# Performance work log

Measured on AMD Instinct MI355X. Metric: run time of the kernel, lower is better.

## Reference

```python
import jax, jax.numpy as jnp
import numpy as np
import math

MAX_T = 1000

def _timestep_emb(t, emb_dim):
    half = emb_dim // 2
    freqs = jnp.exp(jnp.arange(half, dtype=jnp.float32) * -(math.log(MAX_T) / (half - 1)))
    e = t.astype(jnp.float32)[:, None] * freqs[None, :]
    return jnp.concatenate([jnp.sin(e), jnp.cos(e)], axis=1)  # [bs, emb_dim]


def setup_inputs() -> dict:
    key = jax.random.key(0)
    ks = jax.random.split(key, 12)
    BS, N, D, H = 16, 1024, 128, 8  # batch, nodes(=in_channels), out_dim(=d), heads
    w = lambda k, shape: jax.random.normal(k, shape, dtype=jnp.float32) * 0.05
    return {
        "A_t": jax.random.normal(ks[0], (BS, N, N), dtype=jnp.float32),
        "F_c": jax.random.normal(ks[1], (BS, N, D), dtype=jnp.float32),
        "t": jax.random.randint(ks[2], (BS,), 0, MAX_T),
        "Wq": w(ks[3], (D, D * H)), "bq": jnp.zeros((D * H,), jnp.float32),
        "Wk": w(ks[4], (D, D * H)), "bk": jnp.zeros((D * H,), jnp.float32),
        "Wv": w(ks[5], (D, D * H)), "bv": jnp.zeros((D * H,), jnp.float32),
        "Wo": w(ks[6], (D * H, D)), "bo": jnp.zeros((D,), jnp.float32),
        "Wg": jnp.eye(D, dtype=jnp.float32),  # GCN weight, eye init
    }


def reference(A_t, F_c, t, Wq, bq, Wk, bk, Wv, bv, Wo, bo, Wg):
    BS, N, D = F_c.shape
    H = Wq.shape[1] // D
    # timestep embedding, emb_dim = in_channels = N
    t_emb = _timestep_emb(t, N)                       # [bs, N]
    c = F_c + t_emb[:, :, None]                       # [bs, N, D]
    # naive multi-head self-attention with per-head dim = out_dim
    q = (c @ Wq + bq).reshape(BS, N, H, D).transpose(0, 2, 1, 3)
    k = (c @ Wk + bk).reshape(BS, N, H, D).transpose(0, 2, 1, 3)
    v = (c @ Wv + bv).reshape(BS, N, H, D).transpose(0, 2, 1, 3)
    scores = jnp.einsum('bhnd,bhmd->bhnm', q, k) / math.sqrt(D)
    a = jax.nn.softmax(scores, axis=-1)
    ctx = jnp.einsum('bhnm,bhmd->bhnd', a, v)
    ctx = ctx.transpose(0, 2, 1, 3).reshape(BS, N, H * D)
    h = ctx @ Wo + bo                                 # [bs, N, D]
    # GCN: relu(A @ (h @ W))
    feat = jax.nn.relu(A_t @ (h @ Wg))                # [bs, N, D]
    # Corr: row-normalize (unbiased std, matching torch.std) then bmm
    mu = feat.mean(axis=-1, keepdims=True)
    std = jnp.std(feat, axis=-1, ddof=1, keepdims=True)
    norm = (feat - mu) / (std + 1e-8)
    return jnp.einsum('bnd,bmd->bnm', norm, norm) / feat.shape[-1]
```

## Files before the change

kernel.cpp:

```cpp
#include <hip/hip_runtime.h>
#include <math.h>

#define NN 1024
#define DD 128
#define HH 8

typedef __attribute__((ext_vector_type(8))) short short8;
typedef __attribute__((ext_vector_type(4))) float f32x4;

__device__ inline unsigned short f2bf(float x) {
    union { float f; unsigned u; } v; v.f = x;
    return (unsigned short)((v.u + 0x7FFF + ((v.u >> 16) & 1)) >> 16);
}
__device__ inline unsigned pack2(float a, float b) {
    return (unsigned)f2bf(a) | ((unsigned)f2bf(b) << 16);
}

__global__ __launch_bounds__(256) void k_prep_w(
    const float* __restrict__ Wq, const float* __restrict__ Wk, const float* __restrict__ Wv,
    const float* __restrict__ Wo, const float* __restrict__ Wg,
    unsigned short* WqT, unsigned short* WkT, unsigned short* WvT,
    unsigned short* WoT, unsigned short* WgT) {
    int id = blockIdx.x;
    const float* src; unsigned short* dst; int R, C, ti;
    if (id < 128)      { src = Wq; dst = WqT; R = 128;  C = 1024; ti = id; }
    else if (id < 256) { src = Wk; dst = WkT; R = 128;  C = 1024; ti = id - 128; }
    else if (id < 384) { src = Wv; dst = WvT; R = 128;  C = 1024; ti = id - 256; }
    else if (id < 512) { src = Wo; dst = WoT; R = 1024; C = 128;  ti = id - 384; }
    else               { src = Wg; dst = WgT; R = 128;  C = 128;  ti = id - 512; }
    int tc = C >> 5;
    int r0 = (ti / tc) << 5, c0 = (ti % tc) << 5;
    __shared__ float T[32][33];
    int tid = threadIdx.x;
    int r = tid >> 3, c4 = (tid & 7) << 2;
    float4 v = *(const float4*)&src[(size_t)(r0 + r) * C + c0 + c4];
    T[r][c4] = v.x; T[r][c4 + 1] = v.y; T[r][c4 + 2] = v.z; T[r][c4 + 3] = v.w;
    __syncthreads();
    int c = tid >> 3, r4 = (tid & 7) << 2;
    uint2 o;
    o.x = pack2(T[r4][c], T[r4 + 1][c]);
    o.y = pack2(T[r4 + 2][c], T[r4 + 3][c]);
    *(uint2*)&dst[(size_t)(c0 + c) * R + r0 + r4] = o;
}

__global__ __launch_bounds__(256) void k_embed(const float* __restrict__ F_c,
                                               const int* __restrict__ t,
                                               unsigned short* __restrict__ cb) {
    int gi = blockIdx.x * 256 + threadIdx.x;
    int row = gi >> 4, ch = gi & 15;
    int b = row >> 10, n = row & 1023;
    float tv = (float)t[b];
    int j = n & 511;
    float e = tv * expf(-(float)j * 0.013518112092919054f);
    float emb = (n < 512) ? sinf(e) : cosf(e);
    const float* src = F_c + (size_t)row * 128 + ch * 8;
    float4 a = *(const float4*)src;
    float4 c4 = *(const float4*)(src + 4);
    uint4 o;
    o.x = pack2(a.x + emb, a.y + emb);  o.y = pack2(a.z + emb, a.w + emb);
    o.z = pack2(c4.x + emb, c4.y + emb); o.w = pack2(c4.z + emb, c4.w + emb);
    *(uint4*)&cb[(size_t)row * 128 + ch * 8] = o;
}

__device__ __forceinline__ void proj_body(const unsigned short* __restrict__ Ain,
                                          const unsigned short* __restrict__ WT,
                                          const float* __restrict__ bias,
                                          unsigned short* __restrict__ Out,
                                          float scale, int mode, int bh_mul,
                                          unsigned short* sm, int head, int m0) {
    unsigned short* CT  = sm;
    unsigned short* WTs = sm + 128 * 136;
    int tid = threadIdx.x;
    int w = tid >> 6, lane = tid & 63, n16 = lane & 15, quad = lane >> 4;
#pragma unroll
    for (int p = 0; p < 8; ++p) {
        int idx = tid + p * 256;
        int r = idx >> 4, ch = idx & 15;
        *(uint4*)&CT[r * 136 + ch * 8]  = *(const uint4*)&Ain[(size_t)(m0 + r) * 128 + ch * 8];
        *(uint4*)&WTs[r * 136 + ch * 8] = *(const uint4*)&WT[(size_t)(head * 128 + r) * 128 + ch * 8];
    }
    __syncthreads();
    int wr = (w >> 1) * 64, wc = (w & 1) * 64;
    f32x4 acc[4][4];
#pragma unroll
    for (int i = 0; i < 4; i++)
#pragma unroll
        for (int j = 0; j < 4; j++) acc[i][j] = (f32x4){0.f, 0.f, 0.f, 0.f};
#pragma unroll
    for (int kk = 0; kk < 4; ++kk) {
        short8 af[4], bf[4];
#pragma unroll
        for (int rb = 0; rb < 4; ++rb)
            af[rb] = *(const short8*)&CT[(wr + rb * 16 + n16) * 136 + kk * 32 + quad * 8];
#pragma unroll
        for (int cb = 0; cb < 4; ++cb)
            bf[cb] = *(const short8*)&WTs[(wc + cb * 16 + n16) * 136 + kk * 32 + quad * 8];
#pragma unroll
        for (int rb = 0; rb < 4; ++rb)
#pragma unroll
            for (int cb = 0; cb < 4; ++cb)
                acc[rb][cb] = __builtin_amdgcn_mfma_f32_16x16x32_bf16(af[rb], bf[cb], acc[rb][cb], 0, 0, 0);
    }
    __syncthreads();
#pragma unroll
    for (int rb = 0; rb < 4; ++rb)
#pragma unroll
        for (int cb = 0; cb < 4; ++cb) {
            int colb = wc + cb * 16 + n16;
            float bs = bias ? bias[head * 128 + colb] : 0.f;
#pragma unroll
            for (int reg = 0; reg < 4; ++reg) {
                int rowb = wr + rb * 16 + quad * 4 + reg;
                unsigned short val = f2bf((acc[rb][cb][reg] + bs) * scale);
                if (mode == 0) CT[rowb * 136 + colb] = val;
                else           CT[colb * 136 + rowb] = val;
            }
        }
    __syncthreads();
    int b = m0 >> 10, n0 = m0 & 1023;
    size_t base = (size_t)(b * bh_mul + head) * 131072;
    if (mode == 0) {
#pragma unroll
        for (int p = 0; p < 8; ++p) {
            int idx = tid + p * 256;
            int r = idx >> 4, ch = idx & 15;
            *(uint4*)&Out[base + (size_t)(n0 + r) * 128 + ch * 8] = *(const uint4*)&CT[r * 136 + ch * 8];
        }
    } else {
#pragma unroll
        for (int p = 0; p < 8; ++p) {
            int idx = tid + p * 256;
            int r = idx >> 4, ch = idx & 15;
            *(uint4*)&Out[base + (size_t)r * 1024 + n0 + ch * 8] = *(const uint4*)&CT[r * 136 + ch * 8];
        }
    }
}

__global__ __launch_bounds__(256) void k_proj_qkv(const unsigned short* __restrict__ Ain,
                                                  const unsigned short* __restrict__ W0,
                                                  const unsigned short* __restrict__ W1,
                                                  const unsigned short* __restrict__ W2,
                                                  const float* __restrict__ b0,
                                                  const float* __restrict__ b1,
                                                  const float* __restrict__ b2,
                                                  unsigned short* __restrict__ O0,
                                                  unsigned short* __restrict__ O1,
                                                  unsigned short* __restrict__ O2,
                                                  float qscale) {
    __shared__ __align__(16) unsigned short sm[2 * 128 * 136];
    int z = blockIdx.z;
    const unsigned short* WT = (z == 0) ? W0 : (z == 1) ? W1 : W2;
    const float* bias = (z == 0) ? b0 : (z == 1) ? b1 : b2;
    unsigned short* Out = (z == 0) ? O0 : (z == 1) ? O1 : O2;
    float scale = (z == 0) ? qscale : 1.f;
    int mode = (z == 2) ? 1 : 0;
    proj_body(Ain, WT, bias, Out, scale, mode, 8, sm, blockIdx.y, blockIdx.x * 128);
}

__global__ __launch_bounds__(256) void k_proj(const unsigned short* __restrict__ Ain,
                                              const unsigned short* __restrict__ WT,
                                              const float* __restrict__ bias,
                                              unsigned short* __restrict__ Out,
                                              float scale, int mode, int bh_mul) {
    __shared__ __align__(16) unsigned short sm[2 * 128 * 136];
    proj_body(Ain, WT, bias, Out, scale, mode, bh_mul, sm, blockIdx.y, blockIdx.x * 128);
}

__device__ __forceinline__ void attn_compute(const unsigned short* __restrict__ Ksc,
                                             const unsigned short* __restrict__ Vtc,
                                             const short8 (&qf)[2][4],
                                             float (&mrun)[2], float (&lrun)[2],
                                             f32x4 (&O)[2][8], int n16, int quad) {
    f32x4 S[2][4];
#pragma unroll
    for (int qb2 = 0; qb2 < 2; ++qb2)
#pragma unroll
        for (int kb = 0; kb < 4; ++kb) S[qb2][kb] = (f32x4){0.f, 0.f, 0.f, 0.f};
    __builtin_amdgcn_s_setprio(1);
#pragma unroll
    for (int kb = 0; kb < 4; ++kb)
#pragma unroll
        for (int dc = 0; dc < 4; ++dc) {
            short8 kf = *(const short8*)&Ksc[(kb * 16 + n16) * 136 + dc * 32 + quad * 8];
            S[0][kb] = __builtin_amdgcn_mfma_f32_16x16x32_bf16(kf, qf[0][dc], S[0][kb], 0, 0, 0);
            S[1][kb] = __builtin_amdgcn_mfma_f32_16x16x32_bf16(kf, qf[1][dc], S[1][kb], 0, 0, 0);
        }
    __builtin_amdgcn_s_setprio(0);

    float mx[2];
#pragma unroll
    for (int qb2 = 0; qb2 < 2; ++qb2) {
        float m = S[qb2][0][0];
#pragma unroll
        for (int kb = 0; kb < 4; ++kb)
#pragma unroll
            for (int reg = 0; reg < 4; ++reg) m = fmaxf(m, S[qb2][kb][reg]);
        m = fmaxf(m, __shfl_xor(m, 16));
        m = fmaxf(m, __shfl_xor(m, 32));
        mx[qb2] = m;
    }
    int keep = (mx[0] - mrun[0] <= 1.f) && (mx[1] - mrun[1] <= 1.f);
    if (!__all(keep)) {
        float mn0 = fmaxf(mrun[0], mx[0]);
        float mn1 = fmaxf(mrun[1], mx[1]);
        float a0 = __expf(mrun[0] - mn0);
        float a1 = __expf(mrun[1] - mn1);
        mrun[0] = mn0; mrun[1] = mn1;
        lrun[0] *= a0; lrun[1] *= a1;
        float av0[4], av1[4];
#pragma unroll
        for (int reg = 0; reg < 4; ++reg) {
            av0[reg] = __shfl(a0, quad * 4 + reg);
            av1[reg] = __shfl(a1, quad * 4 + reg);
        }
#pragma unroll
        for (int dc = 0; dc < 8; ++dc)
#pragma unroll
            for (int reg = 0; reg < 4; ++reg) {
                O[0][dc][reg] *= av0[reg];
                O[1][dc][reg] *= av1[reg];
            }
    }
#pragma unroll
    for (int qb2 = 0; qb2 < 2; ++qb2) {
        float ps = 0.f;
#pragma unroll
        for (int kb = 0; kb < 4; ++kb)
#pragma unroll
            for (int reg = 0; reg < 4; ++reg) {
                float p = __expf(S[qb2][kb][reg] - mrun[qb2]);
                S[qb2][kb][reg] = p;
                ps += p;
            }
        ps += __shfl_xor(ps, 16);
        ps += __shfl_xor(ps, 32);
        lrun[qb2] += ps;
    }
    unsigned pk01[2][4], pk23[2][4];
#pragma unroll
    for (int qb2 = 0; qb2 < 2; ++qb2)
#pragma unroll
        for (int kb = 0; kb < 4; ++kb) {
            asm("v_cvt_pk_bf16_f32 %0, %1, %2"
                : "=v"(pk01[qb2][kb]) : "v"(S[qb2][kb][0]), "v"(S[qb2][kb][1]));
            asm("v_cvt_pk_bf16_f32 %0, %1, %2"
                : "=v"(pk23[qb2][kb]) : "v"(S[qb2][kb][2]), "v"(S[qb2][kb][3]));
        }
    __builtin_amdgcn_s_setprio(1);
#pragma unroll
    for (int c = 0; c < 2; ++c) {
        union { uint4 u; short8 s; } pa0, pa1;
        pa0.u = make_uint4(pk01[0][2 * c], pk23[0][2 * c], pk01[0][2 * c + 1], pk23[0][2 * c + 1]);
        pa1.u = make_uint4(pk01[1][2 * c], pk23[1][2 * c], pk01[1][2 * c + 1], pk23[1][2 * c + 1]);
#pragma unroll
        for (int dc = 0; dc < 8; ++dc) {
            short8 vf = *(const short8*)&Vtc[(dc * 16 + n16) * 72 + c * 32 + quad * 8];
            O[0][dc] = __builtin_amdgcn_mfma_f32_16x16x32_bf16(pa0.s, vf, O[0][dc], 0, 0, 0);
            O[1][dc] = __builtin_amdgcn_mfma_f32_16x16x32_bf16(pa1.s, vf, O[1][dc], 0, 0, 0);
        }
    }
    __builtin_amdgcn_s_setprio(0);
}

__global__ __launch_bounds__(256, 2) void k_attn2(const unsigned short* __restrict__ qbuf,
                                                  const unsigned short* __restrict__ kbuf,
                                                  const unsigned short* __restrict__ vtb,
                                                  unsigned short* __restrict__ ctxb) {
    __shared__ __align__(16) unsigned short sm[35840];
    const int tid = threadIdx.x;
    const int w = tid >> 6, lane = tid & 63;
    const int n16 = lane & 15, quad = lane >> 4;
    const int g = blockIdx.x;
    const int bh = g & 127, tileq = g >> 7;

    const unsigned short* Qp = qbuf + (size_t)bh * 131072 + (size_t)tileq * 16384;
    const unsigned short* Kp = kbuf + (size_t)bh * 131072;
    const unsigned short* Vp = vtb + (size_t)bh * 131072;

    short8 qf[2][4];
#pragma unroll
    for (int qb2 = 0; qb2 < 2; ++qb2)
#pragma unroll
        for (int dc = 0; dc < 4; ++dc)
            qf[qb2][dc] = *(const short8*)&Qp[(size_t)(w * 32 + qb2 * 16 + n16) * 128 + dc * 32 + quad * 8];

    float mrun[2] = {-1e30f, -1e30f};
    float lrun[2] = {0.f, 0.f};
    f32x4 O[2][8];
#pragma unroll
    for (int qb2 = 0; qb2 < 2; ++qb2)
#pragma unroll
        for (int dc = 0; dc < 8; ++dc) O[qb2][dc] = (f32x4){0.f, 0.f, 0.f, 0.f};

    const int vr0 = tid >> 3;
    const int k0 = (tid & 7) * 8;
    const int slotA = ((k0 >> 5) << 5) | (((k0 >> 2) & 3) << 3) | (((k0 >> 4) & 1) << 2);

    uint4 ka[4], va[4];
#pragma unroll
    for (int p = 0; p < 4; ++p) {
        int idx = tid + p * 256;
        int r = idx >> 4, ch = idx & 15;
        ka[p] = *(const uint4*)&Kp[(size_t)r * 128 + ch * 8];
        va[p] = *(const uint4*)&Vp[(size_t)(vr0 + p * 32) * 1024 + k0];
    }
    {
        unsigned short* Kw = sm;
        unsigned short* Vw = sm + 8704;
#pragma unroll
        for (int p = 0; p < 4; ++p) {
            int idx = tid + p * 256;
            int r = idx >> 4, ch = idx & 15;
            *(uint4*)&Kw[r * 136 + ch * 8] = ka[p];
        }
#pragma unroll
        for (int p = 0; p < 4; ++p) {
            int r = vr0 + p * 32;
            *(uint2*)&Vw[r * 72 + slotA]     = make_uint2(va[p].x, va[p].y);
            *(uint2*)&Vw[r * 72 + slotA + 8] = make_uint2(va[p].z, va[p].w);
        }
    }
    __syncthreads();

    for (int kt = 0; kt < 16; ++kt) {
        if (kt < 15) {
#pragma unroll
            for (int p = 0; p < 4; ++p) {
                int idx = tid + p * 256;
                int r = idx >> 4, ch = idx & 15;
                ka[p] = *(const uint4*)&Kp[(size_t)((kt + 1) * 64 + r) * 128 + ch * 8];
                va[p] = *(const uint4*)&Vp[(size_t)(vr0 + p * 32) * 1024 + (kt + 1) * 64 + k0];
            }
        }
        {
            const unsigned short* Ksc = sm + (kt & 1) * 17920;
            const unsigned short* Vtc = Ksc + 8704;
            attn_compute(Ksc, Vtc, qf, mrun, lrun, O, n16, quad);
        }
        if (kt < 15) {
            unsigned short* Kw = sm + ((kt + 1) & 1) * 17920;
            unsigned short* Vw = Kw + 8704;
#pragma unroll
            for (int p = 0; p < 4; ++p) {
                int idx = tid + p * 256;
                int r = idx >> 4, ch = idx & 15;
                *(uint4*)&Kw[r * 136 + ch * 8] = ka[p];
            }
#pragma unroll
            for (int p = 0; p < 4; ++p) {
                int r = vr0 + p * 32;
                *(uint2*)&Vw[r * 72 + slotA]     = make_uint2(va[p].x, va[p].y);
                *(uint2*)&Vw[r * 72 + slotA + 8] = make_uint2(va[p].z, va[p].w);
            }
        }
        __syncthreads();
    }

    float lv[2][4];
#pragma unroll
    for (int qb2 = 0; qb2 < 2; ++qb2)
#pragma unroll
        for (int reg = 0; reg < 4; ++reg)
            lv[qb2][reg] = 1.f / __shfl(lrun[qb2], quad * 4 + reg);
    unsigned short* Ct = sm;
#pragma unroll
    for (int qb2 = 0; qb2 < 2; ++qb2)
#pragma unroll
        for (int reg = 0; reg < 4; ++reg) {
            int row = w * 32 + qb2 * 16 + quad * 4 + reg;
#pragma unroll
            for (int dc = 0; dc < 8; ++dc)
                Ct[row * 136 + dc * 16 + n16] = f2bf(O[qb2][dc][reg] * lv[qb2][reg]);
        }
    __syncthreads();
    unsigned short* Outp = ctxb + (size_t)bh * 131072 + (size_t)tileq * 16384;
#pragma unroll
    for (int p = 0; p < 8; ++p) {
        int idx = tid + p * 256;
        int r = idx >> 4, ch = idx & 15;
        *(uint4*)&Outp[(size_t)r * 128 + ch * 8] = *(const uint4*)&Ct[r * 136 + ch * 8];
    }
}

__global__ __launch_bounds__(256) void k_proj_o(const unsigned short* __restrict__ Ctxb,
                                                const unsigned short* __restrict__ WoT,
                                                const float* __restrict__ bo,
                                                unsigned short* __restrict__ Hb) {
    __shared__ __align__(16) unsigned short sm[64 * 72 + 128 * 72];
    unsigned short* As = sm;
    unsigned short* Bs = sm + 64 * 72;
    int tid = threadIdx.x;
    int m0 = blockIdx.x * 64;
    int b = m0 >> 10, n0 = m0 & 1023;
    int w = tid >> 6, lane = tid & 63, n16 = lane & 15, quad = lane >> 4;
    int wr = (w & 1) * 32, wc = (w >> 1) * 64;
    f32x4 acc[2][4];
#pragma unroll
    for (int i = 0; i < 2; i++)
#pragma unroll
        for (int j = 0; j < 4; j++) acc[i][j] = (f32x4){0.f, 0.f, 0.f, 0.f};
    for (int kt = 0; kt < 16; ++kt) {
        __syncthreads();
        int hh = kt >> 1, d0 = (kt & 1) * 64;
#pragma unroll
        for (int p = 0; p < 2; ++p) {
            int idx = tid + p * 256;
            int r = idx >> 3, ch = idx & 7;
            *(uint4*)&As[r * 72 + ch * 8] =
                *(const uint4*)&Ctxb[((size_t)(b * 8 + hh) * 1024 + n0 + r) * 128 + d0 + ch * 8];
        }
#pragma unroll
        for (int p = 0; p < 4; ++p) {
            int idx = tid + p * 256;
            int r = idx >> 3, ch = idx & 7;
            *(uint4*)&Bs[r * 72 + ch * 8] = *(const uint4*)&WoT[(size_t)r * 1024 + kt * 64 + ch * 8];
        }
        __syncthreads();
#pragma unroll
        for (int kk = 0; kk < 2; ++kk) {
            short8 af0 = *(const short8*)&As[(wr + n16) * 72 + kk * 32 + quad * 8];
            short8 af1 = *(const short8*)&As[(wr + 16 + n16) * 72 + kk * 32 + quad * 8];
#pragma unroll
            for (int cb = 0; cb < 4; ++cb) {
                short8 bf = *(const short8*)&Bs[(wc + cb * 16 + n16) * 72 + kk * 32 + quad * 8];
                acc[0][cb] = __builtin_amdgcn_mfma_f32_16x16x32_bf16(af0, bf, acc[0][cb], 0, 0, 0);
                acc[1][cb] = __builtin_amdgcn_mfma_f32_16x16x32_bf16(af1, bf, acc[1][cb], 0, 0, 0);
            }
        }
    }
    __syncthreads();
    unsigned short* Ct = sm;
#pragma unroll
    for (int rb = 0; rb < 2; ++rb)
#pragma unroll
        for (int cb = 0; cb < 4; ++cb) {
            int col = wc + cb * 16 + n16;
            float bs = bo[col];
#pragma unroll
            for (int reg = 0; reg < 4; ++reg)
                Ct[(wr + rb * 16 + quad * 4 + reg) * 136 + col] = f2bf(acc[rb][cb][reg] + bs);
        }
    __syncthreads();
#pragma unroll
    for (int p = 0; p < 4; ++p) {
        int idx = tid + p * 256;
        int r = idx >> 4, ch = idx & 15;
        *(uint4*)&Hb[(size_t)(m0 + r) * 128 + ch * 8] = *(const uint4*)&Ct[r * 136 + ch * 8];
    }
}

__global__ __launch_bounds__(256) void k_at_gemm(const float* __restrict__ At,
                                                 const unsigned short* __restrict__ HgT,
                                                 float* __restrict__ Feat) {
    __shared__ __align__(16) unsigned short sm[64 * 72 + 128 * 72];
    unsigned short* As = sm;
    unsigned short* Bs = sm + 64 * 72;
    int tid = threadIdx.x;
    int bz = blockIdx.z;
    int m0 = blockIdx.x * 64;
    int w = tid >> 6, lane = tid & 63, n16 = lane & 15, quad = lane >> 4;
    int wr = (w & 1) * 32, wc = (w >> 1) * 64;
    f32x4 acc[2][4];
#pragma unroll
    for (int i = 0; i < 2; i++)
#pragma unroll
        for (int j = 0; j < 4; j++) acc[i][j] = (f32x4){0.f, 0.f, 0.f, 0.f};
    for (int kt = 0; kt < 16; ++kt) {
        __syncthreads();
#pragma unroll
        for (int p = 0; p < 2; ++p) {
            int idx = tid + p * 256;
            int r = idx >> 3, ch = idx & 7;
            const float* s = At + (size_t)bz * 1048576 + (size_t)(m0 + r) * 1024 + kt * 64 + ch * 8;
            float4 x = *(const float4*)s;
            float4 y = *(const float4*)(s + 4);
            uint4 o;
            o.x = pack2(x.x, x.y); o.y = pack2(x.z, x.w);
            o.z = pack2(y.x, y.y); o.w = pack2(y.z, y.w);
            *(uint4*)&As[r * 72 + ch * 8] = o;
        }
#pragma unroll
        for (int p = 0; p < 4; ++p) {
            int idx = tid + p * 256;
            int r = idx >> 3, ch = idx & 7;
            *(uint4*)&Bs[r * 72 + ch * 8] =
                *(const uint4*)&HgT[(size_t)bz * 131072 + (size_t)r * 1024 + kt * 64 + ch * 8];
        }
        __syncthreads();
#pragma unroll
        for (int kk = 0; kk < 2; ++kk) {
            short8 af0 = *(const short8*)&As[(wr + n16) * 72 + kk * 32 + quad * 8];
            short8 af1 = *(const short8*)&As[(wr + 16 + n16) * 72 + kk * 32 + quad * 8];
#pragma unroll
            for (int cb = 0; cb < 4; ++cb) {
                short8 bf = *(const short8*)&Bs[(wc + cb * 16 + n16) * 72 + kk * 32 + quad * 8];
                acc[0][cb] = __builtin_amdgcn_mfma_f32_16x16x32_bf16(af0, bf, acc[0][cb], 0, 0, 0);
                acc[1][cb] = __builtin_amdgcn_mfma_f32_16x16x32_bf16(af1, bf, acc[1][cb], 0, 0, 0);
            }
        }
    }
#pragma unroll
    for (int rb = 0; rb < 2; ++rb)
#pragma unroll
        for (int cb = 0; cb < 4; ++cb) {
            int col = wc + cb * 16 + n16;
#pragma unroll
            for (int reg = 0; reg < 4; ++reg) {
                int row = m0 + wr + rb * 16 + quad * 4 + reg;
                Feat[(size_t)bz * 131072 + (size_t)row * 128 + col] = fmaxf(acc[rb][cb][reg], 0.f);
            }
        }
}

__global__ __launch_bounds__(64) void k_norm(const float* __restrict__ F,
                                             unsigned short* __restrict__ Nb) {
    int row = blockIdx.x, tdx = threadIdx.x;
    const float* p = F + (size_t)row * 128;
    float2 xy = *(const float2*)&p[tdx * 2];
    float sum = xy.x + xy.y;
#pragma unroll
    for (int off = 32; off; off >>= 1) sum += __shfl_xor(sum, off);
    float mu = sum * (1.f / 128.f);
    float d0 = xy.x - mu, d1 = xy.y - mu;
    float sq = d0 * d0 + d1 * d1;
#pragma unroll
    for (int off = 32; off; off >>= 1) sq += __shfl_xor(sq, off);
    float sd = sqrtf(sq * (1.f / 127.f));
    float inv = 1.f / (sd + 1e-8f);
    ((unsigned*)Nb)[(size_t)row * 64 + tdx] = pack2(d0 * inv, d1 * inv);
}

__global__ __launch_bounds__(256) void k_corr(const unsigned short* __restrict__ Nb,
                                              float* __restrict__ Out) {
    __shared__ __align__(16) unsigned short sm[2 * 128 * 136];
    unsigned short* Ar = sm;
    unsigned short* Br = sm + 128 * 136;
    int tid = threadIdx.x;
    int bz = blockIdx.z;
    int n0 = blockIdx.x * 128, m0 = blockIdx.y * 128;
    const unsigned short* base = Nb + (size_t)bz * 131072;
    int w = tid >> 6, lane = tid & 63, n16 = lane & 15, quad = lane >> 4;
#pragma unroll
    for (int p = 0; p < 8; ++p) {
        int idx = tid + p * 256;
        int r = idx >> 4, ch = idx & 15;
        *(uint4*)&Ar[r * 136 + ch * 8] = *(const uint4*)&base[(size_t)(n0 + r) * 128 + ch * 8];
        *(uint4*)&Br[r * 136 + ch * 8] = *(const uint4*)&base[(size_t)(m0 + r) * 128 + ch * 8];
    }
    __syncthreads();
    int wr = (w >> 1) * 64, wc = (w & 1) * 64;
    f32x4 acc[4][4];
#pragma unroll
    for (int i = 0; i < 4; i++)
#pragma unroll
        for (int j = 0; j < 4; j++) acc[i][j] = (f32x4){0.f, 0.f, 0.f, 0.f};
#pragma unroll
    for (int kk = 0; kk < 4; ++kk) {
        short8 af[4], bf[4];
#pragma unroll
        for (int rb = 0; rb < 4; ++rb)
            af[rb] = *(const short8*)&Ar[(wr + rb * 16 + n16) * 136 + kk * 32 + quad * 8];
#pragma unroll
        for (int cb = 0; cb < 4; ++cb)
            bf[cb] = *(const short8*)&Br[(wc + cb * 16 + n16) * 136 + kk * 32 + quad * 8];
#pragma unroll
        for (int rb = 0; rb < 4; ++rb)
#pragma unroll
            for (int cb = 0; cb < 4; ++cb)
                acc[rb][cb] = __builtin_amdgcn_mfma_f32_16x16x32_bf16(af[rb], bf[cb], acc[rb][cb], 0, 0, 0);
    }
#pragma unroll
    for (int rb = 0; rb < 4; ++rb)
#pragma unroll
        for (int cb = 0; cb < 4; ++cb)
#pragma unroll
            for (int reg = 0; reg < 4; ++reg) {
                int row = n0 + wr + rb * 16 + quad * 4 + reg;
                int col = m0 + wc + cb * 16 + n16;
                Out[(size_t)bz * 1048576 + (size_t)row * 1024 + col] = acc[rb][cb][reg] * 0.0078125f;
            }
}

extern "C" void kernel_launch(void* const* d_in, const int* in_sizes, int n_in,
                              void* d_out, int out_size, void* d_ws, size_t ws_size,
                              hipStream_t stream) {
    const float* A_t = (const float*)d_in[0];
    const float* F_c = (const float*)d_in[1];
    const int*   t   = (const int*)d_in[2];
    const float* Wq  = (const float*)d_in[3];
    const float* bq  = (const float*)d_in[4];
    const float* Wk  = (const float*)d_in[5];
    const float* bk  = (const float*)d_in[6];
    const float* Wv  = (const float*)d_in[7];
    const float* bv  = (const float*)d_in[8];
    const float* Wo  = (const float*)d_in[9];
    const float* bo  = (const float*)d_in[10];
    const float* Wg  = (const float*)d_in[11];
    float* out = (float*)d_out;
    char* ws = (char*)d_ws;

    unsigned short* cb   = (unsigned short*)(ws);
    unsigned short* qb   = (unsigned short*)(ws + 4194304);
    unsigned short* kbuf = (unsigned short*)(ws + 37748736);
    unsigned short* vtb  = (unsigned short*)(ws + 71303168);
    unsigned short* ctxb = (unsigned short*)(ws + 104857600);
    unsigned short* hb   = (unsigned short*)(ws + 138412032);
    unsigned short* hgT  = (unsigned short*)(ws + 142606336);
    float*          feat = (float*)        (ws + 146800640);
    unsigned short* nb   = (unsigned short*)(ws + 155189248);
    unsigned short* WqT  = (unsigned short*)(ws + 159383552);
    unsigned short* WkT  = (unsigned short*)(ws + 159645696);
    unsigned short* WvT  = (unsigned short*)(ws + 159907840);
    unsigned short* WoT  = (unsigned short*)(ws + 160169984);
    unsigned short* WgT  = (unsigned short*)(ws + 160432128);

    const float qscale = 0.08838834764831845f;

    k_prep_w<<<528, 256, 0, stream>>>(Wq, Wk, Wv, Wo, Wg, WqT, WkT, WvT, WoT, WgT);
    k_embed<<<1024, 256, 0, stream>>>(F_c, t, cb);
    k_proj_qkv<<<dim3(128, 8, 3), 256, 0, stream>>>(cb, WqT, WkT, WvT, bq, bk, bv,
                                                    qb, kbuf, vtb, qscale);
    k_attn2<<<1024, 256, 0, stream>>>(qb, kbuf, vtb, ctxb);
    k_proj_o<<<256, 256, 0, stream>>>(ctxb, WoT, bo, hb);
    k_proj<<<dim3(128, 1), 256, 0, stream>>>(hb, WgT, nullptr, hgT, 1.f, 1, 1);
    k_at_gemm<<<dim3(16, 1, 16), 256, 0, stream>>>(A_t, hgT, feat);
    k_norm<<<16384, 64, 0, stream>>>(feat, nb);
    k_corr<<<dim3(8, 8, 16), 256, 0, stream>>>(nb, out);
}
```

Before: 348.5 us.

## Swizzle attention K/V LDS layout and double-buffer out-proj and adjacency GEMMs

The attention kernel drops padded LDS row strides for K and V^T and uses XOR-swizzled unpadded layouts. This cuts LDS to 64KB per block and is meant to avoid bank conflicts without padding. The output-projection and A_t GEMM kernels gain register-staged double buffering: the next tile's global loads are issued before the current tile's MFMAs, so each k-step needs one barrier instead of two. This doubles their shared memory and adds register pressure, which may cost occupancy.

Result: faster. 321.6 us (-7.7%).

```diff
diff --git a/kernel.cpp b/kernel.cpp
--- a/kernel.cpp
+++ b/kernel.cpp
@@ -171,6 +171,7 @@
                                              const short8 (&qf)[2][4],
                                              float (&mrun)[2], float (&lrun)[2],
                                              f32x4 (&O)[2][8], int n16, int quad) {
+    const int swz = (n16 & 7) << 3;
     f32x4 S[2][4];
 #pragma unroll
     for (int qb2 = 0; qb2 < 2; ++qb2)
@@ -181,7 +182,7 @@
     for (int kb = 0; kb < 4; ++kb)
 #pragma unroll
         for (int dc = 0; dc < 4; ++dc) {
-            short8 kf = *(const short8*)&Ksc[(kb * 16 + n16) * 136 + dc * 32 + quad * 8];
+            short8 kf = *(const short8*)&Ksc[((kb * 16 + n16) << 7) + ((dc * 32 + quad * 8) ^ swz)];
             S[0][kb] = __builtin_amdgcn_mfma_f32_16x16x32_bf16(kf, qf[0][dc], S[0][kb], 0, 0, 0);
             S[1][kb] = __builtin_amdgcn_mfma_f32_16x16x32_bf16(kf, qf[1][dc], S[1][kb], 0, 0, 0);
         }
@@ -254,7 +255,7 @@
         pa1.u = make_uint4(pk01[1][2 * c], pk23[1][2 * c], pk01[1][2 * c + 1], pk23[1][2 * c + 1]);
 #pragma unroll
         for (int dc = 0; dc < 8; ++dc) {
-            short8 vf = *(const short8*)&Vtc[(dc * 16 + n16) * 72 + c * 32 + quad * 8];
+            short8 vf = *(const short8*)&Vtc[((dc * 16 + n16) << 6) + ((c * 32 + quad * 8) ^ swz)];
             O[0][dc] = __builtin_amdgcn_mfma_f32_16x16x32_bf16(pa0.s, vf, O[0][dc], 0, 0, 0);
             O[1][dc] = __builtin_amdgcn_mfma_f32_16x16x32_bf16(pa1.s, vf, O[1][dc], 0, 0, 0);
         }
@@ -266,7 +267,7 @@
                                                   const unsigned short* __restrict__ kbuf,
                                                   const unsigned short* __restrict__ vtb,
                                                   unsigned short* __restrict__ ctxb) {
-    __shared__ __align__(16) unsigned short sm[35840];
+    __shared__ __align__(16) unsigned short sm[32768];
     const int tid = threadIdx.x;
     const int w = tid >> 6, lane = tid & 63;
     const int n16 = lane & 15, quad = lane >> 4;
@@ -295,29 +296,27 @@
     const int vr0 = tid >> 3;
     const int k0 = (tid & 7) * 8;
     const int slotA = ((k0 >> 5) << 5) | (((k0 >> 2) & 3) << 3) | (((k0 >> 4) & 1) << 2);
+    const int voff = slotA ^ ((vr0 & 7) << 3);
+    const int kr0 = tid >> 4, kch = tid & 15;
+    const int kwoff = ((kch ^ (kr0 & 7)) << 3);
 
     uint4 ka[4], va[4];
 #pragma unroll
     for (int p = 0; p < 4; ++p) {
-        int idx = tid + p * 256;
-        int r = idx >> 4, ch = idx & 15;
-        ka[p] = *(const uint4*)&Kp[(size_t)r * 128 + ch * 8];
+        ka[p] = *(const uint4*)&Kp[(size_t)(kr0 + p * 16) * 128 + kch * 8];
         va[p] = *(const uint4*)&Vp[(size_t)(vr0 + p * 32) * 1024 + k0];
     }
     {
         unsigned short* Kw = sm;
-        unsigned short* Vw = sm + 8704;
+        unsigned short* Vw = sm + 8192;
+#pragma unroll
+        for (int p = 0; p < 4; ++p)
+            *(uint4*)&Kw[((kr0 + p * 16) << 7) + kwoff] = ka[p];
 #pragma unroll
         for (int p = 0; p < 4; ++p) {
-            int idx = tid + p * 256;
-            int r = idx >> 4, ch = idx & 15;
-            *(uint4*)&Kw[r * 136 + ch * 8] = ka[p];
-        }
-#pragma unroll
-        for (int p = 0; p < 4; ++p) {
-            int r = vr0 + p * 32;
-            *(uint2*)&Vw[r * 72 + slotA]     = make_uint2(va[p].x, va[p].y);
-            *(uint2*)&Vw[r * 72 + slotA + 8] = make_uint2(va[p].z, va[p].w);
+            int rb6 = (vr0 + p * 32) << 6;
+            *(uint2*)&Vw[rb6 + voff]       = make_uint2(va[p].x, va[p].y);
+            *(uint2*)&Vw[rb6 + (voff ^ 8)] = make_uint2(va[p].z, va[p].w);
         }
     }
     __syncthreads();
@@ -326,31 +325,26 @@
         if (kt < 15) {
 #pragma unroll
             for (int p = 0; p < 4; ++p) {
-                int idx = tid + p * 256;
-                int r = idx >> 4, ch = idx & 15;
-                ka[p] = *(const uint4*)&Kp[(size_t)((kt + 1) * 64 + r) * 128 + ch * 8];
+                ka[p] = *(const uint4*)&Kp[(size_t)((kt + 1) * 64 + kr0 + p * 16) * 128 + kch * 8];
                 va[p] = *(const uint4*)&Vp[(size_t)(vr0 + p * 32) * 1024 + (kt + 1) * 64 + k0];
             }
         }
         {
-            const unsigned short* Ksc = sm + (kt & 1) * 17920;
-            const unsigned short* Vtc = Ksc + 8704;
+            const unsigned short* Ksc = sm + (kt & 1) * 16384;
+            const unsigned short* Vtc = Ksc + 8192;
             attn_compute(Ksc, Vtc, qf, mrun, lrun, O, n16, quad);
         }
         if (kt < 15) {
-            unsigned short* Kw = sm + ((kt + 1) & 1) * 17920;
-            unsigned short* Vw = Kw + 8704;
+            unsigned short* Kw = sm + ((kt + 1) & 1) * 16384;
+            unsigned short* Vw = Kw + 8192;
+#pragma unroll
+            for (int p = 0; p < 4; ++p)
+                *(uint4*)&Kw[((kr0 + p * 16) << 7) + kwoff] = ka[p];
 #pragma unroll
             for (int p = 0; p < 4; ++p) {
-                int idx = tid + p * 256;
-                int r = idx >> 4, ch = idx & 15;
-                *(uint4*)&Kw[r * 136 + ch * 8] = ka[p];
-            }
-#pragma unroll
-            for (int p = 0; p < 4; ++p) {
-                int r = vr0 + p * 32;
-                *(uint2*)&Vw[r * 72 + slotA]     = make_uint2(va[p].x, va[p].y);
-                *(uint2*)&Vw[r * 72 + slotA + 8] = make_uint2(va[p].z, va[p].w);
+                int rb6 = (vr0 + p * 32) << 6;
+                *(uint2*)&Vw[rb6 + voff]       = make_uint2(va[p].x, va[p].y);
+                *(uint2*)&Vw[rb6 + (voff ^ 8)] = make_uint2(va[p].z, va[p].w);
             }
         }
         __syncthreads();
@@ -386,36 +380,46 @@
                                                 const unsigned short* __restrict__ WoT,
                                                 const float* __restrict__ bo,
                                                 unsigned short* __restrict__ Hb) {
-    __shared__ __align__(16) unsigned short sm[64 * 72 + 128 * 72];
-    unsigned short* As = sm;
-    unsigned short* Bs = sm + 64 * 72;
+    __shared__ __align__(16) unsigned short sm[2 * 13824];
     int tid = threadIdx.x;
     int m0 = blockIdx.x * 64;
     int b = m0 >> 10, n0 = m0 & 1023;
     int w = tid >> 6, lane = tid & 63, n16 = lane & 15, quad = lane >> 4;
     int wr = (w & 1) * 32, wc = (w >> 1) * 64;
+    int r8 = tid >> 3, ch8 = tid & 7;
     f32x4 acc[2][4];
 #pragma unroll
     for (int i = 0; i < 2; i++)
 #pragma unroll
         for (int j = 0; j < 4; j++) acc[i][j] = (f32x4){0.f, 0.f, 0.f, 0.f};
+    uint4 aR[2], bR[4];
+#pragma unroll
+    for (int p = 0; p < 2; ++p)
+        aR[p] = *(const uint4*)&Ctxb[((size_t)(b * 8) * 1024 + n0 + r8 + p * 32) * 128 + ch8 * 8];
+#pragma unroll
+    for (int p = 0; p < 4; ++p)
+        bR[p] = *(const uint4*)&WoT[(size_t)(r8 + p * 32) * 1024 + ch8 * 8];
+    {
+        unsigned short* As = sm;
+        unsigned short* Bs = sm + 64 * 72;
+#pragma unroll
+        for (int p = 0; p < 2; ++p) *(uint4*)&As[(r8 + p * 32) * 72 + ch8 * 8] = aR[p];
+#pragma unroll
+        for (int p = 0; p < 4; ++p) *(uint4*)&Bs[(r8 + p * 32) * 72 + ch8 * 8] = bR[p];
+    }
+    __syncthreads();
     for (int kt = 0; kt < 16; ++kt) {
-        __syncthreads();
-        int hh = kt >> 1, d0 = (kt & 1) * 64;
-#pragma unroll
-        for (int p = 0; p < 2; ++p) {
-            int idx = tid + p * 256;
-            int r = idx >> 3, ch = idx & 7;
-            *(uint4*)&As[r * 72 + ch * 8] =
-                *(const uint4*)&Ctxb[((size_t)(b * 8 + hh) * 1024 + n0 + r) * 128 + d0 + ch * 8];
-        }
-#pragma unroll
-        for (int p = 0; p < 4; ++p) {
-            int idx = tid + p * 256;
-            int r = idx >> 3, ch = idx & 7;
-            *(uint4*)&Bs[r * 72 + ch * 8] = *(const uint4*)&WoT[(size_t)r * 1024 + kt * 64 + ch * 8];
-        }
-        __syncthreads();
+        if (kt < 15) {
+            int kn = kt + 1, hh = kn >> 1, d0 = (kn & 1) * 64;
+#pragma unroll
+            for (int p = 0; p < 2; ++p)
+                aR[p] = *(const uint4*)&Ctxb[((size_t)(b * 8 + hh) * 1024 + n0 + r8 + p * 32) * 128 + d0 + ch8 * 8];
+#pragma unroll
+            for (int p = 0; p < 4; ++p)
+                bR[p] = *(const uint4*)&WoT[(size_t)(r8 + p * 32) * 1024 + kn * 64 + ch8 * 8];
+        }
+        const unsigned short* As = sm + (kt & 1) * 13824;
+        const unsigned short* Bs = As + 64 * 72;
 #pragma unroll
         for (int kk = 0; kk < 2; ++kk) {
             short8 af0 = *(const short8*)&As[(wr + n16) * 72 + kk * 32 + quad * 8];
@@ -427,8 +431,16 @@
                 acc[1][cb] = __builtin_amdgcn_mfma_f32_16x16x32_bf16(af1, bf, acc[1][cb], 0, 0, 0);
             }
         }
-    }
-    __syncthreads();
+        if (kt < 15) {
+            unsigned short* Aw = sm + ((kt + 1) & 1) * 13824;
+            unsigned short* Bw = Aw + 64 * 72;
+#pragma unroll
+            for (int p = 0; p < 2; ++p) *(uint4*)&Aw[(r8 + p * 32) * 72 + ch8 * 8] = aR[p];
+#pragma unroll
+            for (int p = 0; p < 4; ++p) *(uint4*)&Bw[(r8 + p * 32) * 72 + ch8 * 8] = bR[p];
+        }
+        __syncthreads();
+    }
     unsigned short* Ct = sm;
 #pragma unroll
     for (int rb = 0; rb < 2; ++rb)
@@ -452,41 +464,57 @@
 __global__ __launch_bounds__(256) void k_at_gemm(const float* __restrict__ At,
                                                  const unsigned short* __restrict__ HgT,
                                                  float* __restrict__ Feat) {
-    __shared__ __align__(16) unsigned short sm[64 * 72 + 128 * 72];
-    unsigned short* As = sm;
-    unsigned short* Bs = sm + 64 * 72;
+    __shared__ __align__(16) unsigned short sm[2 * 13824];
     int tid = threadIdx.x;
     int bz = blockIdx.z;
     int m0 = blockIdx.x * 64;
     int w = tid >> 6, lane = tid & 63, n16 = lane & 15, quad = lane >> 4;
     int wr = (w & 1) * 32, wc = (w >> 1) * 64;
+    int r8 = tid >> 3, ch8 = tid & 7;
     f32x4 acc[2][4];
 #pragma unroll
     for (int i = 0; i < 2; i++)
 #pragma unroll
         for (int j = 0; j < 4; j++) acc[i][j] = (f32x4){0.f, 0.f, 0.f, 0.f};
+    float4 axR[2], ayR[2]; uint4 bR[4];
+#pragma unroll
+    for (int p = 0; p < 2; ++p) {
+        const float* s = At + (size_t)bz * 1048576 + (size_t)(m0 + r8 + p * 32) * 1024 + ch8 * 8;
+        axR[p] = *(const float4*)s;
+        ayR[p] = *(const float4*)(s + 4);
+    }
+#pragma unroll
+    for (int p = 0; p < 4; ++p)
+        bR[p] = *(const uint4*)&HgT[(size_t)bz * 131072 + (size_t)(r8 + p * 32) * 1024 + ch8 * 8];
+    {
+        unsigned short* As = sm;
+        unsigned short* Bs = sm + 64 * 72;
+#pragma unroll
+        for (int p = 0; p < 2; ++p) {
+            uint4 o;
+            o.x = pack2(axR[p].x, axR[p].y); o.y = pack2(axR[p].z, axR[p].w);
+            o.z = pack2(ayR[p].x, ayR[p].y); o.w = pack2(ayR[p].z, ayR[p].w);
+            *(uint4*)&As[(r8 + p * 32) * 72 + ch8 * 8] = o;
+        }
+#pragma unroll
+        for (int p = 0; p < 4; ++p) *(uint4*)&Bs[(r8 + p * 32) * 72 + ch8 * 8] = bR[p];
+    }
+    __syncthreads();
     for (int kt = 0; kt < 16; ++kt) {
-        __syncthreads();
-#pragma unroll
-        for (int p = 0; p < 2; ++p) {
-            int idx = tid + p * 256;
-            int r = idx >> 3, ch = idx & 7;
-            const float* s = At + (size_t)bz * 1048576 + (size_t)(m0 + r) * 1024 + kt * 64 + ch * 8;
-            float4 x = *(const float4*)s;
-            float4 y = *(const float4*)(s + 4);
-            uint4 o;
-            o.x = pack2(x.x, x.y); o.y = pack2(x.z, x.w);
-            o.z = pack2(y.x, y.y); o.w = pack2(y.z, y.w);
-            *(uint4*)&As[r * 72 + ch * 8] = o;
-        }
-#pragma unroll
-        for (int p = 0; p < 4; ++p) {
-            int idx = tid + p * 256;
-            int r = idx >> 3, ch = idx & 7;
-            *(uint4*)&Bs[r * 72 + ch * 8] =
-                *(const uint4*)&HgT[(size_t)bz * 131072 + (size_t)r * 1024 + kt * 64 + ch * 8];
-        }
-        __syncthreads();
+        if (kt < 15) {
+            int kn = kt + 1;
+#pragma unroll
+            for (int p = 0; p < 2; ++p) {
+                const float* s = At + (size_t)bz * 1048576 + (size_t)(m0 + r8 + p * 32) * 1024 + kn * 64 + ch8 * 8;
+                axR[p] = *(const float4*)s;
+                ayR[p] = *(const float4*)(s + 4);
+            }
+#pragma unroll
+            for (int p = 0; p < 4; ++p)
+                bR[p] = *(const uint4*)&HgT[(size_t)bz * 131072 + (size_t)(r8 + p * 32) * 1024 + kn * 64 + ch8 * 8];
+        }
+        const unsigned short* As = sm + (kt & 1) * 13824;
+        const unsigned short* Bs = As + 64 * 72;
 #pragma unroll
         for (int kk = 0; kk < 2; ++kk) {
             short8 af0 = *(const short8*)&As[(wr + n16) * 72 + kk * 32 + quad * 8];
@@ -498,6 +526,20 @@
                 acc[1][cb] = __builtin_amdgcn_mfma_f32_16x16x32_bf16(af1, bf, acc[1][cb], 0, 0, 0);
             }
         }
+        if (kt < 15) {
+            unsigned short* Aw = sm + ((kt + 1) & 1) * 13824;
+            unsigned short* Bw = Aw + 64 * 72;
+#pragma unroll
+            for (int p = 0; p < 2; ++p) {
+                uint4 o;
+                o.x = pack2(axR[p].x, axR[p].y); o.y = pack2(axR[p].z, axR[p].w);
+                o.z = pack2(ayR[p].x, ayR[p].y); o.w = pack2(ayR[p].z, ayR[p].w);
+                *(uint4*)&Aw[(r8 + p * 32) * 72 + ch8 * 8] = o;
+            }
+#pragma unroll
+            for (int p = 0; p < 4; ++p) *(uint4*)&Bw[(r8 + p * 32) * 72 + ch8 * 8] = bR[p];
+        }
+        __syncthreads();
     }
 #pragma unroll
     for (int rb = 0; rb < 2; ++rb)
```
